# Kernel optimization log

Measured on AMD Instinct MI355X. Metric: run time of the kernel, lower is better.

## Reference

```python
import jax, jax.numpy as jnp
import numpy as np

N, E, D, H, Z = 100000, 1600000, 128, 256, 64


def _gconv(x, src, dst, W, b, n):
    # DGL GraphConv, norm='both': D_in^{-1/2} A D_out^{-1/2} x W + b
    ones = jnp.ones(src.shape, x.dtype)
    deg_out = jnp.clip(jax.ops.segment_sum(ones, src, num_segments=n), 1.0)
    deg_in = jnp.clip(jax.ops.segment_sum(ones, dst, num_segments=n), 1.0)
    h = x * (deg_out ** -0.5)[:, None]          # scale by src out-degree
    agg = jax.ops.segment_sum(h[src], dst, num_segments=n)  # SpMM gather/scatter
    return (agg * (deg_in ** -0.5)[:, None]) @ W + b


def setup_inputs() -> dict:
    key = jax.random.key(0)
    ks = jax.random.split(key, 8)
    return {
        "features": jax.random.normal(ks[0], (N, D), jnp.float32),
        "src": jax.random.randint(ks[1], (E,), 0, N, jnp.int32),
        "dst": jax.random.randint(ks[2], (E,), 0, N, jnp.int32),
        "eps": jax.random.normal(ks[3], (N, Z), jnp.float32),
        "W1": jax.random.normal(ks[4], (D, H), jnp.float32) * (1.0 / np.sqrt(D)),
        "b1": jnp.zeros((H,), jnp.float32),
        "W2": jax.random.normal(ks[5], (H, 2 * Z), jnp.float32) * (1.0 / np.sqrt(H)),
        "b2": jnp.zeros((2 * Z,), jnp.float32),
        "W3": jax.random.normal(ks[6], (Z, D), jnp.float32) * (1.0 / np.sqrt(Z)),
        "b3": jnp.zeros((D,), jnp.float32),
    }


def reference(features, src, dst, eps, W1, b1, W2, b2, W3, b3):
    n = features.shape[0]
    h = jax.nn.relu(_gconv(features, src, dst, W1, b1, n))
    mean_logvar = _gconv(h, src, dst, W2, b2, n)
    mean, log_var = jnp.split(mean_logvar, 2, axis=1)
    z = eps * jnp.exp(0.5 * log_var) + mean  # reparameterization
    recon = _gconv(z, src, dst, W3, b3, n)
    return recon, mean, log_var
```

## Files before the change

kernel.cpp:

```cpp
#include <hip/hip_runtime.h>
#include <math.h>


#define MAXD 64

typedef short short8 __attribute__((ext_vector_type(8)));
typedef float f32x4 __attribute__((ext_vector_type(4)));

__device__ __forceinline__ unsigned short f2bf(float f) {
  union { float f; unsigned u; } c; c.f = f;
  unsigned r = c.u + 0x7FFF + ((c.u >> 16) & 1);
  return (unsigned short)(r >> 16);
}
__device__ __forceinline__ float bf2f(unsigned short b) {
  return __builtin_bit_cast(float, (unsigned)b << 16);
}

__global__ __launch_bounds__(256) void k_hist4(const int* __restrict__ src,
    const int* __restrict__ dst, int* __restrict__ degout, int* __restrict__ cnt,
    int* __restrict__ ebuf, int E) {
  int t = blockIdx.x * 256 + threadIdx.x;
  int e0 = t * 4;
  if (e0 + 4 <= E) {
    int4 s4 = *(const int4*)(src + e0);
    int4 d4 = *(const int4*)(dst + e0);
    atomicAdd(&degout[s4.x], 1);
    atomicAdd(&degout[s4.y], 1);
    atomicAdd(&degout[s4.z], 1);
    atomicAdd(&degout[s4.w], 1);
    int p0 = atomicAdd(&cnt[d4.x], 1);
    int p1 = atomicAdd(&cnt[d4.y], 1);
    int p2 = atomicAdd(&cnt[d4.z], 1);
    int p3 = atomicAdd(&cnt[d4.w], 1);
    if (p0 < MAXD) __builtin_nontemporal_store(s4.x, &ebuf[d4.x * MAXD + p0]);
    if (p1 < MAXD) __builtin_nontemporal_store(s4.y, &ebuf[d4.y * MAXD + p1]);
    if (p2 < MAXD) __builtin_nontemporal_store(s4.z, &ebuf[d4.z * MAXD + p2]);
    if (p3 < MAXD) __builtin_nontemporal_store(s4.w, &ebuf[d4.w * MAXD + p3]);
  } else {
    for (int e = e0; e < E; e++) {
      int s = src[e], d = dst[e];
      atomicAdd(&degout[s], 1);
      int p = atomicAdd(&cnt[d], 1);
      if (p < MAXD) __builtin_nontemporal_store(s, &ebuf[d * MAXD + p]);
    }
  }
}

__global__ __launch_bounds__(256) void k_scale(const int* __restrict__ degout,
    const int* __restrict__ cnt, float* __restrict__ sout,
    float* __restrict__ sin_, int N) {
  int i = blockIdx.x * 256 + threadIdx.x;
  if (i >= N) return;
  int dO = degout[i]; if (dO < 1) dO = 1;
  int dI = cnt[i];    if (dI < 1) dI = 1;
  sout[i] = rsqrtf((float)dO);
  sin_[i] = rsqrtf((float)dI);
}

__global__ __launch_bounds__(256) void k_cvt(const float* __restrict__ in,
    unsigned short* __restrict__ out, int n) {
  int i = (blockIdx.x * 256 + threadIdx.x) * 4;
  if (i >= n) return;
  float4 f = *(const float4*)(in + i);
  unsigned lo = (unsigned)f2bf(f.x) | ((unsigned)f2bf(f.y) << 16);
  unsigned hi = (unsigned)f2bf(f.z) | ((unsigned)f2bf(f.w) << 16);
  uint2 o; o.x = lo; o.y = hi;
  *(uint2*)(out + i) = o;
}

template <int K, int OC>
__global__ __launch_bounds__(256) void k_wrepack(const float* __restrict__ W,
    short* __restrict__ Wp) {
  constexpr int KC = K / 32;
  constexpr int TOT = (OC / 16) * KC * 64;
  int t = blockIdx.x * 256 + threadIdx.x;
  if (t >= TOT) return;
  int lane = t & 63;
  int kc = (t >> 6) % KC;
  int nt = t / (KC * 64);
  int n = nt * 16 + (lane & 15);
  int k0 = kc * 32 + ((lane >> 4) * 8);
  short8 v;
  #pragma unroll
  for (int j = 0; j < 8; j++) v[j] = (short)f2bf(W[(size_t)(k0 + j) * OC + n]);
  *(short8*)(Wp + (size_t)t * 8) = v;
}

template <int K, int OC, bool RELU, bool BIAS, bool OUTBF16>
__global__ __launch_bounds__(256) void k_gemm_mfma(
    const unsigned short* __restrict__ A, const short* __restrict__ Wp,
    const float* __restrict__ bias, void* __restrict__ Cout, int N) {
  constexpr int KC = K / 32;
  constexpr int NT = OC / 16;
  int lane = threadIdx.x & 63;
  int wv = threadIdx.x >> 6;
  int m0 = (blockIdx.x * 4 + wv) * 16;
  if (m0 >= N) return;
  int mrow = m0 + (lane & 15);
  if (mrow >= N) mrow = N - 1;
  int q = lane >> 4;
  short8 av[KC];
  #pragma unroll
  for (int kc = 0; kc < KC; kc++)
    av[kc] = *(const short8*)(A + (size_t)mrow * K + kc * 32 + q * 8);
  int col0 = lane & 15;
  int rbase = m0 + q * 4;
  #pragma unroll
  for (int nt = 0; nt < NT; nt++) {
    f32x4 acc = {0.f, 0.f, 0.f, 0.f};
    #pragma unroll
    for (int kc = 0; kc < KC; kc++) {
      short8 bv = *(const short8*)(Wp + ((size_t)(nt * KC + kc) * 64 + lane) * 8);
      acc = __builtin_amdgcn_mfma_f32_16x16x32_bf16(av[kc], bv, acc, 0, 0, 0);
    }
    int col = nt * 16 + col0;
    float bb = BIAS ? bias[col] : 0.f;
    #pragma unroll
    for (int r = 0; r < 4; r++) {
      int row = rbase + r;
      if (row < N) {
        float v = acc[r] + bb;
        if (RELU) v = fmaxf(v, 0.f);
        if (OUTBF16) ((unsigned short*)Cout)[(size_t)row * OC + col] = f2bf(v);
        else         ((float*)Cout)[(size_t)row * OC + col] = v;
      }
    }
  }
}

__global__ __launch_bounds__(256) void k_spmm128b(const unsigned short* __restrict__ x,
    const int* __restrict__ ebuf, const int* __restrict__ cnt,
    const float* __restrict__ sout, const float* __restrict__ sin_,
    unsigned short* __restrict__ out, int N) {
  int lane = threadIdx.x & 63;
  int v = blockIdx.x * 4 + (threadIdx.x >> 6);
  if (v >= N) return;
  v = __builtin_amdgcn_readfirstlane(v);
  int c = cnt[v]; c = c < MAXD ? c : MAXD;
  const int* el = ebuf + (size_t)v * MAXD;
  int u_l = 0; float w_l = 0.f;
  if (lane < c) { u_l = el[lane]; w_l = sout[u_l]; }
  float ax = 0.f, ay = 0.f;
  int i = 0;
  for (; i + 4 <= c; i += 4) {
    #pragma unroll
    for (int j = 0; j < 4; j++) {
      int u = __shfl(u_l, i + j);
      float w = __shfl(w_l, i + j);
      unsigned p = *(const unsigned*)(x + (size_t)u * 128 + lane * 2);
      float lo = __builtin_bit_cast(float, p << 16);
      float hi = __builtin_bit_cast(float, p & 0xFFFF0000u);
      ax = fmaf(w, lo, ax); ay = fmaf(w, hi, ay);
    }
  }
  for (; i < c; i++) {
    int u = __shfl(u_l, i);
    float w = __shfl(w_l, i);
    unsigned p = *(const unsigned*)(x + (size_t)u * 128 + lane * 2);
    float lo = __builtin_bit_cast(float, p << 16);
    float hi = __builtin_bit_cast(float, p & 0xFFFF0000u);
    ax = fmaf(w, lo, ax); ay = fmaf(w, hi, ay);
  }
  float sv = sin_[v];
  unsigned o = (unsigned)f2bf(sv * ax) | ((unsigned)f2bf(sv * ay) << 16);
  *(unsigned*)(out + (size_t)v * 128 + lane * 2) = o;
}

__global__ __launch_bounds__(256) void k_spmm2b(const unsigned short* __restrict__ hw,
    const int* __restrict__ ebuf, const int* __restrict__ cnt,
    const float* __restrict__ sout, const float* __restrict__ sin_,
    const float* __restrict__ b2, const float* __restrict__ eps,
    float* __restrict__ mean_out, float* __restrict__ logvar_out,
    unsigned short* __restrict__ z, int N) {
  int lane = threadIdx.x & 63;
  int v = blockIdx.x * 4 + (threadIdx.x >> 6);
  if (v >= N) return;
  v = __builtin_amdgcn_readfirstlane(v);
  int c = cnt[v]; c = c < MAXD ? c : MAXD;
  const int* el = ebuf + (size_t)v * MAXD;
  int u_l = 0; float w_l = 0.f;
  if (lane < c) { u_l = el[lane]; w_l = sout[u_l]; }
  float ax = 0.f, ay = 0.f;
  int i = 0;
  for (; i + 4 <= c; i += 4) {
    #pragma unroll
    for (int j = 0; j < 4; j++) {
      int u = __shfl(u_l, i + j);
      float w = __shfl(w_l, i + j);
      unsigned p = *(const unsigned*)(hw + (size_t)u * 128 + lane * 2);
      float lo = __builtin_bit_cast(float, p << 16);
      float hi = __builtin_bit_cast(float, p & 0xFFFF0000u);
      ax = fmaf(w, lo, ax); ay = fmaf(w, hi, ay);
    }
  }
  for (; i < c; i++) {
    int u = __shfl(u_l, i);
    float w = __shfl(w_l, i);
    unsigned p = *(const unsigned*)(hw + (size_t)u * 128 + lane * 2);
    float lo = __builtin_bit_cast(float, p << 16);
    float hi = __builtin_bit_cast(float, p & 0xFFFF0000u);
    ax = fmaf(w, lo, ax); ay = fmaf(w, hi, ay);
  }
  float sv = sin_[v];
  float2 bb = ((const float2*)b2)[lane];
  float mx = fmaf(sv, ax, bb.x);
  float my = fmaf(sv, ay, bb.y);
  if (lane < 32) ((float2*)mean_out)[(size_t)v * 32 + lane] = make_float2(mx, my);
  else           ((float2*)logvar_out)[(size_t)v * 32 + (lane - 32)] = make_float2(mx, my);
  float lx = __shfl(mx, (lane & 31) + 32);
  float ly = __shfl(my, (lane & 31) + 32);
  if (lane < 32) {
    float2 e2 = ((const float2*)eps)[(size_t)v * 32 + lane];
    float zx = fmaf(e2.x, expf(0.5f * lx), mx);
    float zy = fmaf(e2.y, expf(0.5f * ly), my);
    unsigned o = (unsigned)f2bf(zx) | ((unsigned)f2bf(zy) << 16);
    *(unsigned*)(z + (size_t)v * 64 + lane * 2) = o;
  }
}

__global__ __launch_bounds__(256) void k_spmm64b(const unsigned short* __restrict__ z,
    const int* __restrict__ ebuf, const int* __restrict__ cnt,
    const float* __restrict__ sout, const float* __restrict__ sin_,
    unsigned short* __restrict__ aggz, int N) {
  int lane = threadIdx.x & 63;
  int v = blockIdx.x * 4 + (threadIdx.x >> 6);
  if (v >= N) return;
  v = __builtin_amdgcn_readfirstlane(v);
  int c = cnt[v]; c = c < MAXD ? c : MAXD;
  const int* el = ebuf + (size_t)v * MAXD;
  int u_l = 0; float w_l = 0.f;
  if (lane < c) { u_l = el[lane]; w_l = sout[u_l]; }
  float a = 0.f;
  int i = 0;
  for (; i + 8 <= c; i += 8) {
    #pragma unroll
    for (int j = 0; j < 8; j++) {
      int u = __shfl(u_l, i + j);
      float w = __shfl(w_l, i + j);
      a = fmaf(w, bf2f(z[(size_t)u * 64 + lane]), a);
    }
  }
  for (; i < c; i++) {
    int u = __shfl(u_l, i);
    float w = __shfl(w_l, i);
    a = fmaf(w, bf2f(z[(size_t)u * 64 + lane]), a);
  }
  aggz[(size_t)v * 64 + lane] = f2bf(sin_[v] * a);
}

extern "C" void kernel_launch(void* const* d_in, const int* in_sizes, int n_in,
                              void* d_out, int out_size, void* d_ws, size_t ws_size,
                              hipStream_t stream) {
  const float* features = (const float*)d_in[0];
  const int*   src      = (const int*)d_in[1];
  const int*   dst      = (const int*)d_in[2];
  const float* eps      = (const float*)d_in[3];
  const float* W1       = (const float*)d_in[4];
  const float* b1       = (const float*)d_in[5];
  const float* W2       = (const float*)d_in[6];
  const float* b2       = (const float*)d_in[7];
  const float* W3       = (const float*)d_in[8];
  const float* b3       = (const float*)d_in[9];
  const int E = in_sizes[1];
  const int N = in_sizes[3] / 64;
  float* out = (float*)d_out;

  char* ws = (char*)d_ws;
  int* degout = (int*)ws;            ws += (size_t)N * 4;
  int* cnt    = (int*)ws;            ws += (size_t)N * 4;
  int* ebuf   = (int*)ws;            ws += (size_t)N * MAXD * 4;
  float* sout = (float*)ws;          ws += (size_t)N * 4;
  float* sin_ = (float*)ws;          ws += (size_t)N * 4;
  short* W1p  = (short*)ws;          ws += 128 * 256 * 2;
  short* W2p  = (short*)ws;          ws += 256 * 128 * 2;
  short* W3p  = (short*)ws;          ws += 64 * 128 * 2;
  char* R1    = ws;                  ws += (size_t)N * 256;
  char* R2    = ws;                  ws += (size_t)N * 256;

  unsigned short* xb    = (unsigned short*)R1;
  unsigned short* hwb   = (unsigned short*)R1;
  unsigned short* aggzb = (unsigned short*)R1;
  unsigned short* agg1b = (unsigned short*)R2;
  unsigned short* zb    = (unsigned short*)R2;

  unsigned short* h     = (unsigned short*)out;
  float* recon          = out;
  float* mean_out       = out + (size_t)N * 128;
  float* logvar_out     = out + (size_t)N * 192;

  hipMemsetAsync(degout, 0, (size_t)N * 8, stream);

  k_hist4<<<((E + 3) / 4 + 255) / 256, 256, 0, stream>>>(src, dst, degout, cnt, ebuf, E);
  k_scale<<<(N + 255) / 256, 256, 0, stream>>>(degout, cnt, sout, sin_, N);
  k_cvt<<<((N * 128 / 4) + 255) / 256, 256, 0, stream>>>(features, xb, N * 128);
  k_wrepack<128, 256><<<16, 256, 0, stream>>>(W1, W1p);
  k_wrepack<256, 128><<<16, 256, 0, stream>>>(W2, W2p);
  k_wrepack<64, 128><<<4, 256, 0, stream>>>(W3, W3p);

  k_spmm128b<<<(N + 3) / 4, 256, 0, stream>>>(xb, ebuf, cnt, sout, sin_, agg1b, N);
  k_gemm_mfma<128, 256, true, true, true>
      <<<(N + 63) / 64, 256, 0, stream>>>(agg1b, W1p, b1, h, N);

  k_gemm_mfma<256, 128, false, false, true>
      <<<(N + 63) / 64, 256, 0, stream>>>(h, W2p, nullptr, hwb, N);
  k_spmm2b<<<(N + 3) / 4, 256, 0, stream>>>(hwb, ebuf, cnt, sout, sin_, b2, eps,
                                            mean_out, logvar_out, zb, N);

  k_spmm64b<<<(N + 3) / 4, 256, 0, stream>>>(zb, ebuf, cnt, sout, sin_, aggzb, N);
  k_gemm_mfma<64, 128, false, true, false>
      <<<(N + 63) / 64, 256, 0, stream>>>(aggzb, W3p, b3, recon, N);
}
```

Baseline: 588.8 us.

## Pre-bucket edges by destination range before building per-node adjacency lists

Replaces the single-pass histogram/scatter of edges into per-destination lists with a two-pass scheme. The first pass partitions edges into 8 coarse destination-range buckets using LDS counters and one global atomic per bucket per block. The second pass fills the per-node ebuf from each bucket, so that scattered atomics and stores land in a smaller, more cache-resident address range. This adds an extra read and write of all edges (8 bytes each) into a scratch region reused from R2, and edges beyond the bucket capacity would be dropped.

Result: slower. 611.6 us (+3.9%).

```diff
diff --git a/kernel.cpp b/kernel.cpp
--- a/kernel.cpp
+++ b/kernel.cpp
@@ -3,6 +3,7 @@
 
 
 #define MAXD 64
+#define NB 8
 
 typedef short short8 __attribute__((ext_vector_type(8)));
 typedef float f32x4 __attribute__((ext_vector_type(4)));
@@ -16,33 +17,71 @@
   return __builtin_bit_cast(float, (unsigned)b << 16);
 }
 
-__global__ __launch_bounds__(256) void k_hist4(const int* __restrict__ src,
-    const int* __restrict__ dst, int* __restrict__ degout, int* __restrict__ cnt,
-    int* __restrict__ ebuf, int E) {
-  int t = blockIdx.x * 256 + threadIdx.x;
-  int e0 = t * 4;
-  if (e0 + 4 <= E) {
+__global__ __launch_bounds__(256) void k_bucket(const int* __restrict__ src,
+    const int* __restrict__ dst, int* __restrict__ degout, int* __restrict__ bcnt,
+    unsigned long long* __restrict__ bkt, int E, float bscale, int cap) {
+  __shared__ int lc[4][NB];
+  __shared__ int lb[4][NB];
+  int tid = threadIdx.x;
+  int wv = tid >> 6;
+  if (tid < 4 * NB) ((int*)lc)[tid] = 0;
+  __syncthreads();
+
+  int e0 = (blockIdx.x * 256 + tid) * 4;
+  int nv = E - e0; nv = nv < 0 ? 0 : (nv > 4 ? 4 : nv);
+  int s[4], d[4], b[4], p[4];
+  if (nv == 4) {
     int4 s4 = *(const int4*)(src + e0);
     int4 d4 = *(const int4*)(dst + e0);
-    atomicAdd(&degout[s4.x], 1);
-    atomicAdd(&degout[s4.y], 1);
-    atomicAdd(&degout[s4.z], 1);
-    atomicAdd(&degout[s4.w], 1);
-    int p0 = atomicAdd(&cnt[d4.x], 1);
-    int p1 = atomicAdd(&cnt[d4.y], 1);
-    int p2 = atomicAdd(&cnt[d4.z], 1);
-    int p3 = atomicAdd(&cnt[d4.w], 1);
-    if (p0 < MAXD) __builtin_nontemporal_store(s4.x, &ebuf[d4.x * MAXD + p0]);
-    if (p1 < MAXD) __builtin_nontemporal_store(s4.y, &ebuf[d4.y * MAXD + p1]);
-    if (p2 < MAXD) __builtin_nontemporal_store(s4.z, &ebuf[d4.z * MAXD + p2]);
-    if (p3 < MAXD) __builtin_nontemporal_store(s4.w, &ebuf[d4.w * MAXD + p3]);
+    s[0] = s4.x; s[1] = s4.y; s[2] = s4.z; s[3] = s4.w;
+    d[0] = d4.x; d[1] = d4.y; d[2] = d4.z; d[3] = d4.w;
   } else {
-    for (int e = e0; e < E; e++) {
-      int s = src[e], d = dst[e];
-      atomicAdd(&degout[s], 1);
-      int p = atomicAdd(&cnt[d], 1);
-      if (p < MAXD) __builtin_nontemporal_store(s, &ebuf[d * MAXD + p]);
-    }
+    for (int j = 0; j < nv; j++) { s[j] = src[e0 + j]; d[j] = dst[e0 + j]; }
+  }
+  #pragma unroll
+  for (int j = 0; j < 4; j++) {
+    if (j < nv) {
+      atomicAdd(&degout[s[j]], 1);
+      int bb = (int)((float)d[j] * bscale);
+      b[j] = bb < NB - 1 ? bb : NB - 1;
+      p[j] = atomicAdd(&lc[wv][b[j]], 1);
+    }
+  }
+  __syncthreads();
+  if (tid < NB) {
+    int t0 = lc[0][tid], t1 = lc[1][tid], t2 = lc[2][tid], t3 = lc[3][tid];
+    int base = atomicAdd(&bcnt[tid], t0 + t1 + t2 + t3);
+    lb[0][tid] = base;
+    lb[1][tid] = base + t0;
+    lb[2][tid] = base + t0 + t1;
+    lb[3][tid] = base + t0 + t1 + t2;
+  }
+  __syncthreads();
+  #pragma unroll
+  for (int j = 0; j < 4; j++) {
+    if (j < nv) {
+      int pos = lb[wv][b[j]] + p[j];
+      if (pos < cap)
+        bkt[(size_t)b[j] * cap + pos] =
+            ((unsigned long long)(unsigned)d[j] << 32) | (unsigned)s[j];
+    }
+  }
+}
+
+__global__ __launch_bounds__(256) void k_fill(
+    const unsigned long long* __restrict__ bkt, const int* __restrict__ bcnt,
+    int* __restrict__ cnt, int* __restrict__ ebuf, int cap) {
+  int b = blockIdx.x & (NB - 1);
+  int cb = blockIdx.x >> 3;
+  int m = bcnt[b]; m = m < cap ? m : cap;
+  const unsigned long long* e = bkt + (size_t)b * cap;
+  int stride = (gridDim.x >> 3) * 256;
+  for (int i = cb * 256 + (int)threadIdx.x; i < m; i += stride) {
+    unsigned long long v = __builtin_nontemporal_load(e + i);
+    int sN = (int)(unsigned)v;
+    int dN = (int)(v >> 32);
+    int p = atomicAdd(&cnt[dN], 1);
+    if (p < MAXD) ebuf[(size_t)dN * MAXD + p] = sN;
   }
 }
 
@@ -268,6 +307,7 @@
   char* ws = (char*)d_ws;
   int* degout = (int*)ws;            ws += (size_t)N * 4;
   int* cnt    = (int*)ws;            ws += (size_t)N * 4;
+  int* bcnt   = (int*)ws;            ws += 32;
   int* ebuf   = (int*)ws;            ws += (size_t)N * MAXD * 4;
   float* sout = (float*)ws;          ws += (size_t)N * 4;
   float* sin_ = (float*)ws;          ws += (size_t)N * 4;
@@ -282,15 +322,19 @@
   unsigned short* aggzb = (unsigned short*)R1;
   unsigned short* agg1b = (unsigned short*)R2;
   unsigned short* zb    = (unsigned short*)R2;
+  unsigned long long* bkt = (unsigned long long*)R2;
+  const int cap = (E + NB - 1) / NB + 4096;
 
   unsigned short* h     = (unsigned short*)out;
   float* recon          = out;
   float* mean_out       = out + (size_t)N * 128;
   float* logvar_out     = out + (size_t)N * 192;
 
-  hipMemsetAsync(degout, 0, (size_t)N * 8, stream);
-
-  k_hist4<<<((E + 3) / 4 + 255) / 256, 256, 0, stream>>>(src, dst, degout, cnt, ebuf, E);
+  hipMemsetAsync(degout, 0, (size_t)N * 8 + 32, stream);
+
+  k_bucket<<<((E + 3) / 4 + 255) / 256, 256, 0, stream>>>(
+      src, dst, degout, bcnt, bkt, E, (float)NB / (float)N, cap);
+  k_fill<<<NB * 128, 256, 0, stream>>>(bkt, bcnt, cnt, ebuf, cap);
   k_scale<<<(N + 255) / 256, 256, 0, stream>>>(degout, cnt, sout, sin_, N);
   k_cvt<<<((N * 128 / 4) + 255) / 256, 256, 0, stream>>>(features, xb, N * 128);
   k_wrepack<128, 256><<<16, 256, 0, stream>>>(W1, W1p);
```

## Replace global-atomic edge histogram with two-pass coarse bucketing and shared-memory CSR build

Applied to the files above, without the earlier changes.

Replaces the single kernel that did global atomics per edge into degree counters and the padded adjacency buffer with a two-level scheme. Edges are first binned by 256-node coarse blocks using shared-memory counters and packed records. Per-block kernels then build the per-node adjacency lists and out-degrees with shared-memory atomics. The aim is to cut contended, scattered global atomics and random writes, at the cost of extra passes, scratch space carved from a reused region, and a fixed per-bucket capacity that could drop edges on skewed graphs.

Result: faster. 541.2 us (-8.1%).

```diff
diff --git a/kernel.cpp b/kernel.cpp
--- a/kernel.cpp
+++ b/kernel.cpp
@@ -3,6 +3,8 @@
 
 
 #define MAXD 64
+#define FBSH 8
+#define EPT  16
 
 typedef short short8 __attribute__((ext_vector_type(8)));
 typedef float f32x4 __attribute__((ext_vector_type(4)));
@@ -16,34 +18,111 @@
   return __builtin_bit_cast(float, (unsigned)b << 16);
 }
 
-__global__ __launch_bounds__(256) void k_hist4(const int* __restrict__ src,
-    const int* __restrict__ dst, int* __restrict__ degout, int* __restrict__ cnt,
-    int* __restrict__ ebuf, int E) {
-  int t = blockIdx.x * 256 + threadIdx.x;
-  int e0 = t * 4;
-  if (e0 + 4 <= E) {
-    int4 s4 = *(const int4*)(src + e0);
-    int4 d4 = *(const int4*)(dst + e0);
-    atomicAdd(&degout[s4.x], 1);
-    atomicAdd(&degout[s4.y], 1);
-    atomicAdd(&degout[s4.z], 1);
-    atomicAdd(&degout[s4.w], 1);
-    int p0 = atomicAdd(&cnt[d4.x], 1);
-    int p1 = atomicAdd(&cnt[d4.y], 1);
-    int p2 = atomicAdd(&cnt[d4.z], 1);
-    int p3 = atomicAdd(&cnt[d4.w], 1);
-    if (p0 < MAXD) __builtin_nontemporal_store(s4.x, &ebuf[d4.x * MAXD + p0]);
-    if (p1 < MAXD) __builtin_nontemporal_store(s4.y, &ebuf[d4.y * MAXD + p1]);
-    if (p2 < MAXD) __builtin_nontemporal_store(s4.z, &ebuf[d4.z * MAXD + p2]);
-    if (p3 < MAXD) __builtin_nontemporal_store(s4.w, &ebuf[d4.w * MAXD + p3]);
-  } else {
-    for (int e = e0; e < E; e++) {
-      int s = src[e], d = dst[e];
-      atomicAdd(&degout[s], 1);
-      int p = atomicAdd(&cnt[d], 1);
-      if (p < MAXD) __builtin_nontemporal_store(s, &ebuf[d * MAXD + p]);
-    }
-  }
+__global__ __launch_bounds__(256) void k_bucket2(const int* __restrict__ src,
+    const int* __restrict__ dst, int* __restrict__ bcd, int* __restrict__ bcs,
+    int* __restrict__ bktd, unsigned char* __restrict__ srec,
+    int E, int NFB, int cap2) {
+  extern __shared__ int sh[];
+  int* lcd = sh;
+  int* lbd = sh + NFB;
+  int* lcs = sh + 2 * NFB;
+  int* lbs = sh + 3 * NFB;
+  int tid = threadIdx.x;
+  for (int i = tid; i < 4 * NFB; i += 256) sh[i] = 0;
+  __syncthreads();
+  int e0 = blockIdx.x * (256 * EPT);
+  #pragma unroll 4
+  for (int j = 0; j < EPT; j++) {
+    int e = e0 + j * 256 + tid;
+    if (e < E) {
+      int d = dst[e]; atomicAdd(&lcd[d >> FBSH], 1);
+      int s = src[e]; atomicAdd(&lcs[s >> FBSH], 1);
+    }
+  }
+  __syncthreads();
+  for (int fb = tid; fb < NFB; fb += 256) {
+    int c = lcd[fb];
+    if (c) lbd[fb] = atomicAdd(&bcd[fb], c);
+    int cs = lcs[fb];
+    if (cs) lbs[fb] = atomicAdd(&bcs[fb], cs);
+  }
+  __syncthreads();
+  #pragma unroll 4
+  for (int j = 0; j < EPT; j++) {
+    int e = e0 + j * 256 + tid;
+    if (e < E) {
+      int d = dst[e]; int s = src[e];
+      int fbd = d >> FBSH;
+      int od = atomicAdd(&lbd[fbd], 1);
+      if (od < cap2) bktd[(size_t)fbd * cap2 + od] = ((d & 255) << 24) | s;
+      int fbs = s >> FBSH;
+      int os = atomicAdd(&lbs[fbs], 1);
+      if (os < cap2) srec[(size_t)fbs * cap2 + os] = (unsigned char)(s & 255);
+    }
+  }
+}
+
+__global__ __launch_bounds__(256) void k_csr(const int* __restrict__ bktd,
+    const int* __restrict__ bcd, int* __restrict__ cnt, int* __restrict__ ebuf,
+    int N, int cap2) {
+  __shared__ int lcnt[256];
+  int fb = blockIdx.x;
+  int tid = threadIdx.x;
+  lcnt[tid] = 0;
+  __syncthreads();
+  int m = bcd[fb]; m = m < cap2 ? m : cap2;
+  const int* rec = bktd + (size_t)fb * cap2;
+  for (int i0 = tid * 4; i0 < m; i0 += 1024) {
+    if (i0 + 4 <= m) {
+      int4 r = *(const int4*)(rec + i0);
+      int dl, s, p;
+      dl = (unsigned)r.x >> 24; s = r.x & 0xFFFFFF;
+      p = atomicAdd(&lcnt[dl], 1);
+      if (p < MAXD) ebuf[((size_t)(fb << FBSH) + dl) * MAXD + p] = s;
+      dl = (unsigned)r.y >> 24; s = r.y & 0xFFFFFF;
+      p = atomicAdd(&lcnt[dl], 1);
+      if (p < MAXD) ebuf[((size_t)(fb << FBSH) + dl) * MAXD + p] = s;
+      dl = (unsigned)r.z >> 24; s = r.z & 0xFFFFFF;
+      p = atomicAdd(&lcnt[dl], 1);
+      if (p < MAXD) ebuf[((size_t)(fb << FBSH) + dl) * MAXD + p] = s;
+      dl = (unsigned)r.w >> 24; s = r.w & 0xFFFFFF;
+      p = atomicAdd(&lcnt[dl], 1);
+      if (p < MAXD) ebuf[((size_t)(fb << FBSH) + dl) * MAXD + p] = s;
+    } else {
+      for (int k = i0; k < m; k++) {
+        int r = rec[k];
+        int dl = (unsigned)r >> 24; int s = r & 0xFFFFFF;
+        int p = atomicAdd(&lcnt[dl], 1);
+        if (p < MAXD) ebuf[((size_t)(fb << FBSH) + dl) * MAXD + p] = s;
+      }
+    }
+  }
+  __syncthreads();
+  int node = (fb << FBSH) + tid;
+  if (node < N) cnt[node] = lcnt[tid];
+}
+
+__global__ __launch_bounds__(256) void k_deg(const unsigned char* __restrict__ srec,
+    const int* __restrict__ bcs, int* __restrict__ degout, int N, int cap2) {
+  __shared__ int lh[256];
+  int fb = blockIdx.x;
+  int tid = threadIdx.x;
+  lh[tid] = 0;
+  __syncthreads();
+  int m = bcs[fb]; m = m < cap2 ? m : cap2;
+  const unsigned char* rec = srec + (size_t)fb * cap2;
+  for (int i0 = tid * 4; i0 < m; i0 += 1024) {
+    if (i0 + 4 <= m) {
+      uchar4 r = *(const uchar4*)(rec + i0);
+      atomicAdd(&lh[r.x], 1); atomicAdd(&lh[r.y], 1);
+      atomicAdd(&lh[r.z], 1); atomicAdd(&lh[r.w], 1);
+    } else {
+      for (int k = i0; k < m; k++) atomicAdd(&lh[rec[k]], 1);
+    }
+  }
+  __syncthreads();
+  int node = (fb << FBSH) + tid;
+  if (node < N) degout[node] = lh[tid];
 }
 
 __global__ __launch_bounds__(256) void k_scale(const int* __restrict__ degout,
@@ -265,9 +344,14 @@
   const int N = in_sizes[3] / 64;
   float* out = (float*)d_out;
 
+  const int NFB = (N + 255) >> FBSH;
+  const int cap2 = ((E / NFB) + 2048 + 255) & ~255;
+
   char* ws = (char*)d_ws;
   int* degout = (int*)ws;            ws += (size_t)N * 4;
   int* cnt    = (int*)ws;            ws += (size_t)N * 4;
+  int* bcd    = (int*)ws;            ws += (size_t)NFB * 4;
+  int* bcs    = (int*)ws;            ws += (size_t)NFB * 4;
   int* ebuf   = (int*)ws;            ws += (size_t)N * MAXD * 4;
   float* sout = (float*)ws;          ws += (size_t)N * 4;
   float* sin_ = (float*)ws;          ws += (size_t)N * 4;
@@ -282,15 +366,21 @@
   unsigned short* aggzb = (unsigned short*)R1;
   unsigned short* agg1b = (unsigned short*)R2;
   unsigned short* zb    = (unsigned short*)R2;
+  int* bktd = (int*)R2;
+  unsigned char* srec = (unsigned char*)(R2 + (size_t)NFB * cap2 * 4);
 
   unsigned short* h     = (unsigned short*)out;
   float* recon          = out;
   float* mean_out       = out + (size_t)N * 128;
   float* logvar_out     = out + (size_t)N * 192;
 
-  hipMemsetAsync(degout, 0, (size_t)N * 8, stream);
-
-  k_hist4<<<((E + 3) / 4 + 255) / 256, 256, 0, stream>>>(src, dst, degout, cnt, ebuf, E);
+  hipMemsetAsync(degout, 0, (size_t)N * 8 + (size_t)NFB * 8, stream);
+
+  const size_t shA = (size_t)4 * NFB * 4;
+  k_bucket2<<<(E + 256 * EPT - 1) / (256 * EPT), 256, shA, stream>>>(
+      src, dst, bcd, bcs, bktd, srec, E, NFB, cap2);
+  k_csr<<<NFB, 256, 0, stream>>>(bktd, bcd, cnt, ebuf, N, cap2);
+  k_deg<<<NFB, 256, 0, stream>>>(srec, bcs, degout, N, cap2);
   k_scale<<<(N + 255) / 256, 256, 0, stream>>>(degout, cnt, sout, sin_, N);
   k_cvt<<<((N * 128 / 4) + 255) / 256, 256, 0, stream>>>(features, xb, N * 128);
   k_wrepack<128, 256><<<16, 256, 0, stream>>>(W1, W1p);
```
